# Optimization experiments

Hardware: AMD Instinct MI355X
Metric: run time of the kernel (lower is better)

## Reference

```python
import jax, jax.numpy as jnp
import numpy as np
from jax import lax

SEQ, B, F, L = 32, 32, 64, 256
OC = 128          # out_channels
K = 5
PAD = (K - 1) // 2
GROUPS = 4 * OC // 32  # GroupNorm groups = 16
EPS = 1e-5


def group_norm(x, w, b):
    # x: (B, C, L); normalize over each group's (C//G, L) slice
    bsz, c, l = x.shape
    xg = x.reshape(bsz, GROUPS, -1)
    mu = jnp.mean(xg, axis=-1, keepdims=True)
    var = jnp.var(xg, axis=-1, keepdims=True)
    xg = (xg - mu) * lax.rsqrt(var + EPS)
    return xg.reshape(bsz, c, l) * w[None, :, None] + b[None, :, None]


def setup_inputs() -> dict:
    key = jax.random.key(0)
    k1, k2, k3 = jax.random.split(key, 3)
    fan_in = (F + OC) * K
    return {
        "inputs": jax.random.normal(k1, (SEQ, B, F, L), dtype=jnp.float32),
        "conv_w": jax.random.normal(k2, (4 * OC, F + OC, K), dtype=jnp.float32) / np.sqrt(fan_in),
        "conv_b": jax.random.normal(k3, (4 * OC,), dtype=jnp.float32) * 0.01,
        "gn_w": jnp.ones((4 * OC,), dtype=jnp.float32),
        "gn_b": jnp.zeros((4 * OC,), dtype=jnp.float32),
    }


def reference(inputs, conv_w, conv_b, gn_w, gn_b):
    bsz, sub_len = inputs.shape[1], inputs.shape[3]
    hx0 = jnp.zeros((bsz, OC, sub_len), dtype=inputs.dtype)
    cx0 = jnp.zeros((bsz, OC, sub_len), dtype=inputs.dtype)

    def step(carry, x):
        hx, cx = carry
        combined = jnp.concatenate([x, hx], axis=1)  # (B, F+OC, L)
        gates = lax.conv_general_dilated(
            combined, conv_w, window_strides=(1,), padding=[(PAD, PAD)],
            dimension_numbers=("NCH", "OIH", "NCH"))
        gates = gates + conv_b[None, :, None]
        gates = group_norm(gates, gn_w, gn_b)
        i, f, g, o = jnp.split(gates, 4, axis=1)
        cy = jax.nn.sigmoid(f) * cx + jax.nn.sigmoid(i) * jnp.tanh(g)
        hy = jax.nn.sigmoid(o) * jnp.tanh(cy)
        return (hy, cy), hy

    (hy, cy), outputs = lax.scan(step, (hx0, cx0), inputs)
    return outputs, (hy, cy)
```

## Files before the change

### kernel.cpp

```cpp
#include <hip/hip_runtime.h>

typedef unsigned short u16;
typedef unsigned int u32;
typedef __attribute__((ext_vector_type(4))) float f32x4;
typedef __attribute__((ext_vector_type(8))) short s16x8;
typedef __attribute__((ext_vector_type(4))) int i32x4;

#define EPS 1e-5f

__device__ __forceinline__ u16 f2bf(float f) {
  unsigned u = __float_as_uint(f);
  return (u16)((u + 0x7fffu + ((u >> 16) & 1u)) >> 16);
}
__device__ __forceinline__ float sigm(float x) { return 1.0f / (1.0f + __expf(-x)); }
__device__ __forceinline__ float tanh_f(float x) {
  float e = __expf(-2.0f * fabsf(x));
  float r = (1.0f - e) / (1.0f + e);
  return copysignf(r, x);
}
__device__ __forceinline__ void gl_lds16(const void* g, void* l) {
  __builtin_amdgcn_global_load_lds(
      (const __attribute__((address_space(1))) u32*)g,
      (__attribute__((address_space(3))) u32*)l, 16, 0, 0);
}

__global__ __launch_bounds__(256) void k_wcvt(const float* __restrict__ w, u16* __restrict__ Wpk) {
  int idx = blockIdx.x * 256 + threadIdx.x;
  int f = idx >> 9, r = idx & 511;
  int lane = r >> 3, j = r & 7;
  int of = f & 31, tk = f >> 5;
  int kk = tk % 6, tap = tk / 6;
  int o = (of << 4) + (lane & 15);
  int c = (kk << 5) + ((lane >> 4) << 3) + j;
  Wpk[idx] = f2bf(w[(o * 192 + c) * 5 + tap]);
}

__global__ __launch_bounds__(256) void k_xtrans(const float* __restrict__ x, u16* __restrict__ xT) {
  int tb = blockIdx.x;
  int tid = threadIdx.x;
  __shared__ __align__(16) u16 ltile[256 * 72];
  const float* src = x + tb * (64 * 256);
  for (int it = 0; it < 64; ++it) {
    int idx = it * 256 + tid;
    int c = idx >> 8, l = idx & 255;
    ltile[l * 72 + c] = f2bf(src[idx]);
  }
  __syncthreads();
  char* dst = (char*)(xT + tb * 16896);
  i32x4 z = {0, 0, 0, 0};
  for (int i = tid; i < 2112; i += 256) {
    int r = i >> 3, ch = i & 7;
    i32x4 v = z;
    if (r >= 2 && r < 258) v = *(const i32x4*)(ltile + (r - 2) * 72 + ch * 8);
    *(i32x4*)(dst + r * 128 + ((ch * 16) ^ ((r & 7) << 4))) = v;
  }
}

__global__ void k_init(i32x4* __restrict__ hT, i32x4* __restrict__ cxv, i32x4* __restrict__ flg) {
  int n = gridDim.x * blockDim.x;
  int tid = blockIdx.x * blockDim.x + threadIdx.x;
  i32x4 z = {0, 0, 0, 0};
  for (int i = tid; i < 270336; i += n) hT[i] = z;
  for (int i = tid; i < 262144; i += n) cxv[i] = z;
  for (int i = tid; i < 2048;   i += n) flg[i] = z;
}

__global__ __launch_bounds__(512) void k_step(
    const u16* __restrict__ Wpk, const u16* __restrict__ xT, u16* __restrict__ hT,
    const float* __restrict__ cb, const float* __restrict__ gnw, const float* __restrict__ gnb,
    float* __restrict__ cx, float* __restrict__ out,
    float* __restrict__ stats, int* __restrict__ flags, int t) {
  int blk = blockIdx.x;
  int b = blk >> 3, cs = (blk >> 1) & 3, lh = blk & 1;
  int tid = threadIdx.x, wave = tid >> 6, lane = tid & 63;
  int wrow = wave & 1, wcol = wave >> 1;

  __shared__ __align__(16) char ldsx[16896];
  __shared__ __align__(16) char ldsh[33792];
  __shared__ __align__(16) char A_lds[4][8192];
  __shared__ __align__(16) char hl[8192];
  __shared__ float red[8][4][2];
  __shared__ float smu[4], srs[4];

  const u16* hTr = hT + (t & 1) * 1081344;
  u16* hTw = hT + ((t + 1) & 1) * 1081344;

  int ofw = ((wave >> 1) << 3) + (cs << 1) + (wave & 1);
  gl_lds16(Wpk + ((ofw << 6) + lane) * 8, A_lds[0] + (wave << 10));
  gl_lds16(Wpk + (((32 + ofw) << 6) + lane) * 8, A_lds[1] + (wave << 10));
  {
    const char* gx = (const char*)(xT + ((t << 5) + b) * 16896 + (lh << 13));
    for (int i = tid; i < 1056; i += 512)
      gl_lds16(gx + (i << 4), ldsx + ((i >> 6) << 10));
    const char* gh = (const char*)(hTr + b * 33792 + (lh << 14));
    for (int i = tid; i < 2112; i += 512)
      gl_lds16(gh + (i << 4), ldsh + ((i >> 6) << 10));
  }
  asm volatile("s_waitcnt vmcnt(0) lgkmcnt(0)" ::: "memory");
  __builtin_amdgcn_s_barrier();

  f32x4 zero4 = {0.f, 0.f, 0.f, 0.f};
  f32x4 acc[4][2];
  #pragma unroll
  for (int g = 0; g < 4; ++g) { acc[g][0] = zero4; acc[g][1] = zero4; }
  int cgrp = (lane >> 4) << 4;

  #pragma unroll
  for (int c = 0; c < 30; ++c) {
    int cn = (c + 2 < 30) ? (c + 2) : 29;
    gl_lds16(Wpk + ((((cn << 5) + ofw) << 6) + lane) * 8, A_lds[(c + 2) & 3] + (wave << 10));
    asm volatile("s_waitcnt vmcnt(2)" ::: "memory");
    __builtin_amdgcn_s_barrier();
    const char* Ab = A_lds[c & 3];
    int tap = c / 6, kk = c % 6;
    s16x8 av[4];
    #pragma unroll
    for (int g = 0; g < 4; ++g)
      av[g] = *(const s16x8*)(Ab + (((g << 1) + wrow) << 10) + (lane << 4));
    s16x8 bv[2];
    #pragma unroll
    for (int ni = 0; ni < 2; ++ni) {
      int row = (wcol << 5) + (ni << 4) + (lane & 15) + tap;
      int sw = (row & 7) << 4;
      const char* p = (kk < 2) ? (ldsx + (row << 7) + (((kk << 6) + cgrp) ^ sw))
                               : (ldsh + (row << 8) + ((((kk - 2) << 6) + cgrp) ^ sw));
      bv[ni] = *(const s16x8*)p;
    }
    #pragma unroll
    for (int g = 0; g < 4; ++g) {
      acc[g][0] = __builtin_amdgcn_mfma_f32_16x16x32_bf16(av[g], bv[0], acc[g][0], 0, 0, 0);
      acc[g][1] = __builtin_amdgcn_mfma_f32_16x16x32_bf16(av[g], bv[1], acc[g][1], 0, 0, 0);
    }
  }

  int ch16 = (lane >> 4) << 2;
  int cbase = (cs << 5) + (wrow << 4) + ch16;
  float sum[4], sq[4];
  #pragma unroll
  for (int g = 0; g < 4; ++g) {
    f32x4 bias = *(const f32x4*)(cb + (g << 7) + cbase);
    sum[g] = 0.f; sq[g] = 0.f;
    #pragma unroll
    for (int ni = 0; ni < 2; ++ni)
      #pragma unroll
      for (int r = 0; r < 4; ++r) {
        float v = acc[g][ni][r] + bias[r];
        acc[g][ni][r] = v;
        sum[g] += v; sq[g] += v * v;
      }
  }
  #pragma unroll
  for (int off = 1; off < 64; off <<= 1) {
    #pragma unroll
    for (int g = 0; g < 4; ++g) {
      sum[g] += __shfl_xor(sum[g], off);
      sq[g]  += __shfl_xor(sq[g], off);
    }
  }
  if (lane == 0) {
    #pragma unroll
    for (int g = 0; g < 4; ++g) { red[wave][g][0] = sum[g]; red[wave][g][1] = sq[g]; }
  }
  __syncthreads();

  int slot = (((t << 5) + b) << 3) + (cs << 1) + lh;
  if (tid == 0) {
    #pragma unroll
    for (int g = 0; g < 4; ++g) {
      float s = 0.f, q = 0.f;
      #pragma unroll
      for (int w = 0; w < 8; ++w) { s += red[w][g][0]; q += red[w][g][1]; }
      __hip_atomic_store(&stats[(slot << 3) + (g << 1)], s, __ATOMIC_RELAXED, __HIP_MEMORY_SCOPE_AGENT);
      __hip_atomic_store(&stats[(slot << 3) + (g << 1) + 1], q, __ATOMIC_RELAXED, __HIP_MEMORY_SCOPE_AGENT);
    }
    __hip_atomic_store(&flags[slot], 1, __ATOMIC_RELEASE, __HIP_MEMORY_SCOPE_AGENT);
    while (__hip_atomic_load(&flags[slot ^ 1], __ATOMIC_ACQUIRE, __HIP_MEMORY_SCOPE_AGENT) == 0) {}
  }
  __syncthreads();
  if (tid < 4) {
    int base = (slot >> 1) << 4;
    float s = __hip_atomic_load(&stats[base + (tid << 1)], __ATOMIC_RELAXED, __HIP_MEMORY_SCOPE_AGENT)
            + __hip_atomic_load(&stats[base + 8 + (tid << 1)], __ATOMIC_RELAXED, __HIP_MEMORY_SCOPE_AGENT);
    float q = __hip_atomic_load(&stats[base + (tid << 1) + 1], __ATOMIC_RELAXED, __HIP_MEMORY_SCOPE_AGENT)
            + __hip_atomic_load(&stats[base + 8 + (tid << 1) + 1], __ATOMIC_RELAXED, __HIP_MEMORY_SCOPE_AGENT);
    const float inv = 1.0f / 8192.0f;
    float m = s * inv;
    smu[tid] = m;
    srs[tid] = rsqrtf(q * inv - m * m + EPS);
  }
  __syncthreads();

  float w4[4][4], b4[4][4], muv[4], rsv[4];
  #pragma unroll
  for (int g = 0; g < 4; ++g) {
    muv[g] = smu[g]; rsv[g] = srs[g];
    #pragma unroll
    for (int r = 0; r < 4; ++r) {
      int c = (g << 7) + cbase + r;
      w4[g][r] = gnw[c]; b4[g][r] = gnb[c];
    }
  }
  float* outp = out + (((t << 5) + b) << 15);
  int lhalf = lane & 15;
  int gran = (wrow << 5) + (ch16 << 1);
  #pragma unroll
  for (int ni = 0; ni < 2; ++ni) {
    int ll = (wcol << 5) + (ni << 4) + lhalf;
    int l = (lh << 7) + ll;
    u16 hp[4];
    #pragma unroll
    for (int r = 0; r < 4; ++r) {
      int c = cbase + r;
      float vi = (acc[0][ni][r] - muv[0]) * rsv[0] * w4[0][r] + b4[0][r];
      float vf = (acc[1][ni][r] - muv[1]) * rsv[1] * w4[1][r] + b4[1][r];
      float vg = (acc[2][ni][r] - muv[2]) * rsv[2] * w4[2][r] + b4[2][r];
      float vo = (acc[3][ni][r] - muv[3]) * rsv[3] * w4[3][r] + b4[3][r];
      int cxi = (((b << 7) + c) << 8) + l;
      float cyv = sigm(vf) * cx[cxi] + sigm(vi) * tanh_f(vg);
      float hyv = sigm(vo) * tanh_f(cyv);
      cx[cxi] = cyv;
      outp[(c << 8) + l] = hyv;
      hp[r] = f2bf(hyv);
      if (t == 31) {
        out[33554432 + cxi] = hyv;
        out[34603008 + cxi] = cyv;
      }
    }
    *(unsigned long long*)(hl + (ll << 6) + (gran ^ ((ll & 3) << 4))) =
        *(const unsigned long long*)hp;
  }
  __syncthreads();

  {
    int ll = tid >> 2, k = tid & 3;
    int row = (lh << 7) + ll + 2;
    i32x4 v = *(const i32x4*)(hl + (ll << 6) + ((k << 4) ^ ((ll & 3) << 4)));
    char* dsth = (char*)hTw + b * 67584 + (row << 8) + ((((cs << 2) + k) << 4) ^ ((row & 7) << 4));
    *(i32x4*)dsth = v;
  }
}

extern "C" void kernel_launch(void* const* d_in, const int* in_sizes, int n_in,
                              void* d_out, int out_size, void* d_ws, size_t ws_size,
                              hipStream_t stream) {
  const float* x  = (const float*)d_in[0];
  const float* cw = (const float*)d_in[1];
  const float* cb = (const float*)d_in[2];
  const float* gw = (const float*)d_in[3];
  const float* gb = (const float*)d_in[4];
  float* out = (float*)d_out;
  char* ws = (char*)d_ws;

  u16*   Wpk   = (u16*)(ws);
  u16*   xT    = (u16*)(ws + 983040);
  u16*   hT    = (u16*)(ws + 35586048);
  float* cx    = (float*)(ws + 39911424);
  float* stats = (float*)(ws + 44105728);
  int*   flags = (int*)(ws + 44367872);

  k_wcvt<<<1920, 256, 0, stream>>>(cw, Wpk);
  k_xtrans<<<1024, 256, 0, stream>>>(x, xT);
  k_init<<<512, 256, 0, stream>>>((i32x4*)hT, (i32x4*)cx, (i32x4*)flags);
  for (int t = 0; t < 32; ++t)
    k_step<<<256, 512, 0, stream>>>(Wpk, xT, hT, cb, gw, gb, cx, out, stats, flags, t);
}
```

Measured before the change: 699.9 us.

## Merge setup kernels, load weights directly to registers, remap block indices

```diff
diff --git a/kernel.cpp b/kernel.cpp
--- a/kernel.cpp
+++ b/kernel.cpp
@@ -2,6 +2,7 @@
 
 typedef unsigned short u16;
 typedef unsigned int u32;
+typedef unsigned long long u64;
 typedef __attribute__((ext_vector_type(4))) float f32x4;
 typedef __attribute__((ext_vector_type(8))) short s16x8;
 typedef __attribute__((ext_vector_type(4))) int i32x4;
@@ -24,45 +25,45 @@
       (__attribute__((address_space(3))) u32*)l, 16, 0, 0);
 }
 
-__global__ __launch_bounds__(256) void k_wcvt(const float* __restrict__ w, u16* __restrict__ Wpk) {
-  int idx = blockIdx.x * 256 + threadIdx.x;
-  int f = idx >> 9, r = idx & 511;
-  int lane = r >> 3, j = r & 7;
-  int of = f & 31, tk = f >> 5;
-  int kk = tk % 6, tap = tk / 6;
-  int o = (of << 4) + (lane & 15);
-  int c = (kk << 5) + ((lane >> 4) << 3) + j;
-  Wpk[idx] = f2bf(w[(o * 192 + c) * 5 + tap]);
-}
-
-__global__ __launch_bounds__(256) void k_xtrans(const float* __restrict__ x, u16* __restrict__ xT) {
-  int tb = blockIdx.x;
-  int tid = threadIdx.x;
+__global__ __launch_bounds__(256) void k_setup(
+    const float* __restrict__ cw, u16* __restrict__ Wpk,
+    const float* __restrict__ x, u16* __restrict__ xT,
+    i32x4* __restrict__ hTz, i32x4* __restrict__ cxz, i32x4* __restrict__ flz) {
+  const int bid = blockIdx.x, tid = threadIdx.x;
   __shared__ __align__(16) u16 ltile[256 * 72];
-  const float* src = x + tb * (64 * 256);
-  for (int it = 0; it < 64; ++it) {
-    int idx = it * 256 + tid;
-    int c = idx >> 8, l = idx & 255;
-    ltile[l * 72 + c] = f2bf(src[idx]);
-  }
-  __syncthreads();
-  char* dst = (char*)(xT + tb * 16896);
-  i32x4 z = {0, 0, 0, 0};
-  for (int i = tid; i < 2112; i += 256) {
-    int r = i >> 3, ch = i & 7;
-    i32x4 v = z;
-    if (r >= 2 && r < 258) v = *(const i32x4*)(ltile + (r - 2) * 72 + ch * 8);
-    *(i32x4*)(dst + r * 128 + ((ch * 16) ^ ((r & 7) << 4))) = v;
-  }
-}
-
-__global__ void k_init(i32x4* __restrict__ hT, i32x4* __restrict__ cxv, i32x4* __restrict__ flg) {
-  int n = gridDim.x * blockDim.x;
-  int tid = blockIdx.x * blockDim.x + threadIdx.x;
-  i32x4 z = {0, 0, 0, 0};
-  for (int i = tid; i < 270336; i += n) hT[i] = z;
-  for (int i = tid; i < 262144; i += n) cxv[i] = z;
-  for (int i = tid; i < 2048;   i += n) flg[i] = z;
+  if (bid < 1920) {
+    int idx = bid * 256 + tid;
+    int f = idx >> 9, r = idx & 511;
+    int lane = r >> 3, j = r & 7;
+    int of = f & 31, tk = f >> 5;
+    int kk = tk % 6, tap = tk / 6;
+    int o = (of << 4) + (lane & 15);
+    int c = (kk << 5) + ((lane >> 4) << 3) + j;
+    Wpk[idx] = f2bf(cw[(o * 192 + c) * 5 + tap]);
+  } else if (bid < 2944) {
+    int tb = bid - 1920;
+    const float* src = x + tb * (64 * 256);
+    for (int it = 0; it < 64; ++it) {
+      int idx = it * 256 + tid;
+      int c = idx >> 8, l = idx & 255;
+      ltile[l * 72 + c] = f2bf(src[idx]);
+    }
+    __syncthreads();
+    char* dst = (char*)(xT + tb * 16896);
+    i32x4 z = {0, 0, 0, 0};
+    for (int i = tid; i < 2112; i += 256) {
+      int r = i >> 3, ch = i & 7;
+      i32x4 v = z;
+      if (r >= 2 && r < 258) v = *(const i32x4*)(ltile + (r - 2) * 72 + ch * 8);
+      *(i32x4*)(dst + r * 128 + ((ch * 16) ^ ((r & 7) << 4))) = v;
+    }
+  } else {
+    int base = (bid - 2944) * 256 + tid;
+    i32x4 z = {0, 0, 0, 0};
+    for (int i = base; i < 270336; i += 131072) hTz[i] = z;
+    for (int i = base; i < 262144; i += 131072) cxz[i] = z;
+    for (int i = base; i < 2048;   i += 131072) flz[i] = z;
+  }
 }
 
 __global__ __launch_bounds__(512) void k_step(
@@ -70,173 +71,180 @@
     const float* __restrict__ cb, const float* __restrict__ gnw, const float* __restrict__ gnb,
     float* __restrict__ cx, float* __restrict__ out,
     float* __restrict__ stats, int* __restrict__ flags, int t) {
-  int blk = blockIdx.x;
-  int b = blk >> 3, cs = (blk >> 1) & 3, lh = blk & 1;
-  int tid = threadIdx.x, wave = tid >> 6, lane = tid & 63;
-  int wrow = wave & 1, wcol = wave >> 1;
+  const int bid = blockIdx.x;
+  const int b = bid & 31, lh = (bid >> 5) & 1, cs = bid >> 6;
+  const int L0 = lh << 7;
+  const int tid = threadIdx.x, wave = tid >> 6, lane = tid & 63;
+  const int wm = wave & 1, wl = wave >> 1;
+  const int l15 = lane & 15, q = lane >> 4;
+  const int cgrp = q << 4;
 
   __shared__ __align__(16) char ldsx[16896];
   __shared__ __align__(16) char ldsh[33792];
-  __shared__ __align__(16) char A_lds[4][8192];
   __shared__ __align__(16) char hl[8192];
   __shared__ float red[8][4][2];
+  __shared__ float blkstat[8];
   __shared__ float smu[4], srs[4];
 
   const u16* hTr = hT + (t & 1) * 1081344;
   u16* hTw = hT + ((t + 1) & 1) * 1081344;
 
-  int ofw = ((wave >> 1) << 3) + (cs << 1) + (wave & 1);
-  gl_lds16(Wpk + ((ofw << 6) + lane) * 8, A_lds[0] + (wave << 10));
-  gl_lds16(Wpk + (((32 + ofw) << 6) + lane) * 8, A_lds[1] + (wave << 10));
   {
-    const char* gx = (const char*)(xT + ((t << 5) + b) * 16896 + (lh << 13));
-    for (int i = tid; i < 1056; i += 512)
-      gl_lds16(gx + (i << 4), ldsx + ((i >> 6) << 10));
-    const char* gh = (const char*)(hTr + b * 33792 + (lh << 14));
-    for (int i = tid; i < 2112; i += 512)
-      gl_lds16(gh + (i << 4), ldsh + ((i >> 6) << 10));
-  }
-  asm volatile("s_waitcnt vmcnt(0) lgkmcnt(0)" ::: "memory");
-  __builtin_amdgcn_s_barrier();
+    const char* gx = (const char*)(xT + ((t << 5) + b) * 16896) + (lh << 14);
+    for (int i = tid; i < 1056; i += 512) gl_lds16(gx + (i << 4), ldsx + (i << 4));
+    const char* gh = (const char*)hTr + b * 67584 + (lh << 15);
+    for (int i = tid; i < 2112; i += 512) gl_lds16(gh + (i << 4), ldsh + (i << 4));
+  }
+  asm volatile("s_waitcnt vmcnt(0)" ::: "memory");
+  __syncthreads();
 
   f32x4 zero4 = {0.f, 0.f, 0.f, 0.f};
   f32x4 acc[4][2];
   #pragma unroll
   for (int g = 0; g < 4; ++g) { acc[g][0] = zero4; acc[g][1] = zero4; }
-  int cgrp = (lane >> 4) << 4;
-
-  #pragma unroll
-  for (int c = 0; c < 30; ++c) {
-    int cn = (c + 2 < 30) ? (c + 2) : 29;
-    gl_lds16(Wpk + ((((cn << 5) + ofw) << 6) + lane) * 8, A_lds[(c + 2) & 3] + (wave << 10));
-    asm volatile("s_waitcnt vmcnt(2)" ::: "memory");
-    __builtin_amdgcn_s_barrier();
-    const char* Ab = A_lds[c & 3];
-    int tap = c / 6, kk = c % 6;
-    s16x8 av[4];
-    #pragma unroll
-    for (int g = 0; g < 4; ++g)
-      av[g] = *(const s16x8*)(Ab + (((g << 1) + wrow) << 10) + (lane << 4));
-    s16x8 bv[2];
-    #pragma unroll
-    for (int ni = 0; ni < 2; ++ni) {
-      int row = (wcol << 5) + (ni << 4) + (lane & 15) + tap;
-      int sw = (row & 7) << 4;
-      const char* p = (kk < 2) ? (ldsx + (row << 7) + (((kk << 6) + cgrp) ^ sw))
-                               : (ldsh + (row << 8) + ((((kk - 2) << 6) + cgrp) ^ sw));
-      bv[ni] = *(const s16x8*)p;
-    }
-    #pragma unroll
-    for (int g = 0; g < 4; ++g) {
-      acc[g][0] = __builtin_amdgcn_mfma_f32_16x16x32_bf16(av[g], bv[0], acc[g][0], 0, 0, 0);
-      acc[g][1] = __builtin_amdgcn_mfma_f32_16x16x32_bf16(av[g], bv[1], acc[g][1], 0, 0, 0);
-    }
-  }
-
-  int ch16 = (lane >> 4) << 2;
-  int cbase = (cs << 5) + (wrow << 4) + ch16;
-  float sum[4], sq[4];
+
+  const s16x8* Wv = (const s16x8*)Wpk;
+  for (int tap = 0; tap < 5; ++tap) {
+    #pragma unroll
+    for (int kk = 0; kk < 6; ++kk) {
+      const int cc = tap * 6 + kk;
+      s16x8 av[4], bv[2];
+      #pragma unroll
+      for (int g = 0; g < 4; ++g) {
+        const int of = (g << 3) + (cs << 1) + wm;
+        av[g] = Wv[(((cc << 5) + of) << 6) + lane];
+      }
+      #pragma unroll
+      for (int ni = 0; ni < 2; ++ni) {
+        const int rr = (wl << 5) + (ni << 4) + l15 + tap;
+        const int sw = (rr & 7) << 4;
+        bv[ni] = (kk < 2)
+          ? *(const s16x8*)(ldsx + (rr << 7) + (((kk << 6) + cgrp) ^ sw))
+          : *(const s16x8*)(ldsh + (rr << 8) + ((((kk - 2) << 6) + cgrp) ^ sw));
+      }
+      #pragma unroll
+      for (int g = 0; g < 4; ++g) {
+        acc[g][0] = __builtin_amdgcn_mfma_f32_16x16x32_bf16(av[g], bv[0], acc[g][0], 0, 0, 0);
+        acc[g][1] = __builtin_amdgcn_mfma_f32_16x16x32_bf16(av[g], bv[1], acc[g][1], 0, 0, 0);
+      }
+    }
+  }
+
+  const int chq = (cs << 5) + (wm << 4) + (q << 2);
+  float sum4[4], sq4[4];
   #pragma unroll
   for (int g = 0; g < 4; ++g) {
-    f32x4 bias = *(const f32x4*)(cb + (g << 7) + cbase);
-    sum[g] = 0.f; sq[g] = 0.f;
+    const f32x4 bias = *(const f32x4*)(cb + (g << 7) + chq);
+    sum4[g] = 0.f; sq4[g] = 0.f;
     #pragma unroll
     for (int ni = 0; ni < 2; ++ni)
       #pragma unroll
       for (int r = 0; r < 4; ++r) {
         float v = acc[g][ni][r] + bias[r];
         acc[g][ni][r] = v;
-        sum[g] += v; sq[g] += v * v;
-      }
+        sum4[g] += v; sq4[g] += v * v;
+      }
+  }
+  f32x4 w4[4], b4[4];
+  float cxv[2][4];
+  #pragma unroll
+  for (int g = 0; g < 4; ++g) {
+    w4[g] = *(const f32x4*)(gnw + (g << 7) + chq);
+    b4[g] = *(const f32x4*)(gnb + (g << 7) + chq);
+  }
+  #pragma unroll
+  for (int ni = 0; ni < 2; ++ni) {
+    const int l = L0 + (wl << 5) + (ni << 4) + l15;
+    #pragma unroll
+    for (int r = 0; r < 4; ++r)
+      cxv[ni][r] = cx[(b << 15) + ((chq + r) << 8) + l];
   }
   #pragma unroll
   for (int off = 1; off < 64; off <<= 1) {
     #pragma unroll
     for (int g = 0; g < 4; ++g) {
-      sum[g] += __shfl_xor(sum[g], off);
-      sq[g]  += __shfl_xor(sq[g], off);
+      sum4[g] += __shfl_xor(sum4[g], off);
+      sq4[g]  += __shfl_xor(sq4[g], off);
     }
   }
   if (lane == 0) {
     #pragma unroll
-    for (int g = 0; g < 4; ++g) { red[wave][g][0] = sum[g]; red[wave][g][1] = sq[g]; }
-  }
-  __syncthreads();
-
-  int slot = (((t << 5) + b) << 3) + (cs << 1) + lh;
+    for (int g = 0; g < 4; ++g) { red[wave][g][0] = sum4[g]; red[wave][g][1] = sq4[g]; }
+  }
+  __syncthreads();
+  if (tid < 8) {
+    const int g = tid >> 1, j = tid & 1;
+    float v = 0.f;
+    #pragma unroll
+    for (int w = 0; w < 8; ++w) v += red[w][g][j];
+    blkstat[tid] = v;
+  }
+  __syncthreads();
+
+  const int sidx = (((t << 5) + b) << 3) + (cs << 1) + lh;
   if (tid == 0) {
+    float* sp = stats + (sidx << 3);
+    #pragma unroll
+    for (int j = 0; j < 8; ++j)
+      __hip_atomic_store(sp + j, blkstat[j], __ATOMIC_RELAXED, __HIP_MEMORY_SCOPE_AGENT);
+    __hip_atomic_store(&flags[sidx], 1, __ATOMIC_RELEASE, __HIP_MEMORY_SCOPE_AGENT);
+    while (__hip_atomic_load(&flags[sidx ^ 1], __ATOMIC_RELAXED, __HIP_MEMORY_SCOPE_AGENT) == 0)
+      __builtin_amdgcn_s_sleep(2);
+    __builtin_amdgcn_fence(__ATOMIC_ACQUIRE, "agent");
+    const float* pe = stats + ((sidx & ~1) << 3);
+    const float* po = stats + ((sidx | 1) << 3);
+    const float inv = 1.0f / 8192.0f;
     #pragma unroll
     for (int g = 0; g < 4; ++g) {
-      float s = 0.f, q = 0.f;
-      #pragma unroll
-      for (int w = 0; w < 8; ++w) { s += red[w][g][0]; q += red[w][g][1]; }
-      __hip_atomic_store(&stats[(slot << 3) + (g << 1)], s, __ATOMIC_RELAXED, __HIP_MEMORY_SCOPE_AGENT);
-      __hip_atomic_store(&stats[(slot << 3) + (g << 1) + 1], q, __ATOMIC_RELAXED, __HIP_MEMORY_SCOPE_AGENT);
-    }
-    __hip_atomic_store(&flags[slot], 1, __ATOMIC_RELEASE, __HIP_MEMORY_SCOPE_AGENT);
-    while (__hip_atomic_load(&flags[slot ^ 1], __ATOMIC_ACQUIRE, __HIP_MEMORY_SCOPE_AGENT) == 0) {}
-  }
-  __syncthreads();
-  if (tid < 4) {
-    int base = (slot >> 1) << 4;
-    float s = __hip_atomic_load(&stats[base + (tid << 1)], __ATOMIC_RELAXED, __HIP_MEMORY_SCOPE_AGENT)
-            + __hip_atomic_load(&stats[base + 8 + (tid << 1)], __ATOMIC_RELAXED, __HIP_MEMORY_SCOPE_AGENT);
-    float q = __hip_atomic_load(&stats[base + (tid << 1) + 1], __ATOMIC_RELAXED, __HIP_MEMORY_SCOPE_AGENT)
-            + __hip_atomic_load(&stats[base + 8 + (tid << 1) + 1], __ATOMIC_RELAXED, __HIP_MEMORY_SCOPE_AGENT);
-    const float inv = 1.0f / 8192.0f;
-    float m = s * inv;
-    smu[tid] = m;
-    srs[tid] = rsqrtf(q * inv - m * m + EPS);
-  }
-  __syncthreads();
-
-  float w4[4][4], b4[4][4], muv[4], rsv[4];
-  #pragma unroll
-  for (int g = 0; g < 4; ++g) {
-    muv[g] = smu[g]; rsv[g] = srs[g];
+      float s = __hip_atomic_load(pe + (g << 1), __ATOMIC_RELAXED, __HIP_MEMORY_SCOPE_AGENT)
+              + __hip_atomic_load(po + (g << 1), __ATOMIC_RELAXED, __HIP_MEMORY_SCOPE_AGENT);
+      float qv = __hip_atomic_load(pe + (g << 1) + 1, __ATOMIC_RELAXED, __HIP_MEMORY_SCOPE_AGENT)
+               + __hip_atomic_load(po + (g << 1) + 1, __ATOMIC_RELAXED, __HIP_MEMORY_SCOPE_AGENT);
+      float m = s * inv;
+      smu[g] = m;
+      srs[g] = rsqrtf(qv * inv - m * m + EPS);
+    }
+  }
+  __syncthreads();
+
+  const float mu0 = smu[0], mu1 = smu[1], mu2 = smu[2], mu3 = smu[3];
+  const float rs0 = srs[0], rs1 = srs[1], rs2 = srs[2], rs3 = srs[3];
+  float* outp = out + (((t << 5) + b) << 15);
+  #pragma unroll
+  for (int ni = 0; ni < 2; ++ni) {
+    const int l = L0 + (wl << 5) + (ni << 4) + l15;
+    const int ll = l - L0;
+    u16 hp[4];
     #pragma unroll
     for (int r = 0; r < 4; ++r) {
-      int c = (g << 7) + cbase + r;
-      w4[g][r] = gnw[c]; b4[g][r] = gnb[c];
-    }
-  }
-  float* outp = out + (((t << 5) + b) << 15);
-  int lhalf = lane & 15;
-  int gran = (wrow << 5) + (ch16 << 1);
-  #pragma unroll
-  for (int ni = 0; ni < 2; ++ni) {
-    int ll = (wcol << 5) + (ni << 4) + lhalf;
-    int l = (lh << 7) + ll;
-    u16 hp[4];
-    #pragma unroll
-    for (int r = 0; r < 4; ++r) {
-      int c = cbase + r;
-      float vi = (acc[0][ni][r] - muv[0]) * rsv[0] * w4[0][r] + b4[0][r];
-      float vf = (acc[1][ni][r] - muv[1]) * rsv[1] * w4[1][r] + b4[1][r];
-      float vg = (acc[2][ni][r] - muv[2]) * rsv[2] * w4[2][r] + b4[2][r];
-      float vo = (acc[3][ni][r] - muv[3]) * rsv[3] * w4[3][r] + b4[3][r];
-      int cxi = (((b << 7) + c) << 8) + l;
-      float cyv = sigm(vf) * cx[cxi] + sigm(vi) * tanh_f(vg);
+      const int c = chq + r;
+      float vi = (acc[0][ni][r] - mu0) * rs0 * w4[0][r] + b4[0][r];
+      float vf = (acc[1][ni][r] - mu1) * rs1 * w4[1][r] + b4[1][r];
+      float vg = (acc[2][ni][r] - mu2) * rs2 * w4[2][r] + b4[2][r];
+      float vo = (acc[3][ni][r] - mu3) * rs3 * w4[3][r] + b4[3][r];
+      float cyv = sigm(vf) * cxv[ni][r] + sigm(vi) * tanh_f(vg);
       float hyv = sigm(vo) * tanh_f(cyv);
-      cx[cxi] = cyv;
-      outp[(c << 8) + l] = hyv;
+      const int ci = (c << 8) + l;
+      cx[(b << 15) + ci] = cyv;
+      outp[ci] = hyv;
       hp[r] = f2bf(hyv);
       if (t == 31) {
-        out[33554432 + cxi] = hyv;
-        out[34603008 + cxi] = cyv;
-      }
-    }
-    *(unsigned long long*)(hl + (ll << 6) + (gran ^ ((ll & 3) << 4))) =
-        *(const unsigned long long*)hp;
+        out[33554432 + (b << 15) + ci] = hyv;
+        out[34603008 + (b << 15) + ci] = cyv;
+      }
+    }
+    *(u64*)(hl + (ll << 6) + (((wm << 5) + (q << 3)) ^ ((ll & 3) << 4))) =
+        *(const u64*)hp;
   }
   __syncthreads();
 
   {
-    int ll = tid >> 2, k = tid & 3;
-    int row = (lh << 7) + ll + 2;
+    const int ll = tid >> 2, k = tid & 3;
+    const int row = L0 + ll + 2;
     i32x4 v = *(const i32x4*)(hl + (ll << 6) + ((k << 4) ^ ((ll & 3) << 4)));
-    char* dsth = (char*)hTw + b * 67584 + (row << 8) + ((((cs << 2) + k) << 4) ^ ((row & 7) << 4));
-    *(i32x4*)dsth = v;
+    char* dst = (char*)hTw + b * 67584 + (row << 8) +
+                ((((cs << 2) + k) << 4) ^ ((row & 7) << 4));
+    *(i32x4*)dst = v;
   }
 }
 
@@ -258,9 +266,7 @@
   float* stats = (float*)(ws + 44105728);
   int*   flags = (int*)(ws + 44367872);
 
-  k_wcvt<<<1920, 256, 0, stream>>>(cw, Wpk);
-  k_xtrans<<<1024, 256, 0, stream>>>(x, xT);
-  k_init<<<512, 256, 0, stream>>>((i32x4*)hT, (i32x4*)cx, (i32x4*)flags);
+  k_setup<<<3456, 256, 0, stream>>>(cw, Wpk, x, xT, (i32x4*)hT, (i32x4*)cx, (i32x4*)flags);
   for (int t = 0; t < 32; ++t)
     k_step<<<256, 512, 0, stream>>>(Wpk, xT, hT, cb, gw, gb, cx, out, stats, flags, t);
 }
```

Measured after the change: 675.0 us. 1.04x faster.
